# Performance work log

Measured on AMD Instinct MI355X. Metric: run time of the kernel, lower is better.

The kernel has to match this reference:

```python
import jax, jax.numpy as jnp
import numpy as np

HEADS = 8
EMBED = 128
HEAD_DIM = EMBED // HEADS


def setup_inputs() -> dict:
    key = jax.random.key(0)
    ks = jax.random.split(key, 6)
    s = 0.05
    return {
        "x": jax.random.normal(ks[0], (8, 128, 128, 128), dtype=jnp.float32),
        "Wq": jax.random.normal(ks[1], (HEAD_DIM, HEAD_DIM), dtype=jnp.float32) * s,
        "Wk": jax.random.normal(ks[2], (HEAD_DIM, HEAD_DIM), dtype=jnp.float32) * s,
        "Wv": jax.random.normal(ks[3], (HEAD_DIM, HEAD_DIM), dtype=jnp.float32) * s,
        "Wo": jax.random.normal(ks[4], (EMBED, EMBED), dtype=jnp.float32) * s,
        "bo": jnp.zeros((EMBED,), dtype=jnp.float32),
    }


def reference(x, Wq, Wk, Wv, Wo, bo):
    # is_width=False: attend along the H axis. x: [N, C, H, W]
    y = jnp.transpose(x, (0, 3, 2, 1))  # [N, W, H, C]
    N, D1, D2, C = y.shape
    y = y.reshape(N * D1, D2, HEADS, HEAD_DIM)  # [n, k, h, d]
    # nn.Linear applies y @ W.T
    q = jnp.einsum("nkhd,ed->nkhe", y, Wq)
    k = jnp.einsum("nkhd,ed->nkhe", y, Wk)
    v = jnp.einsum("nkhd,ed->nkhe", y, Wv)
    energy = jnp.einsum("nqhd,nkhd->nhqk", q, k)
    scale = jnp.asarray(EMBED, energy.dtype) ** 0.5  # note: original divides by sqrt(embed_size)
    attn = jax.nn.softmax(energy / scale, axis=-1)
    out = jnp.einsum("nhqk,nkhd->nqhd", attn, v).reshape(N, D1, D2, C)
    out = jnp.einsum("nqkc,ec->nqke", out, Wo) + bo
    return jnp.transpose(out, (0, 3, 2, 1))  # back to [N, C, H, W]
```

## Files before the change

### kernel.cpp

```cpp
#include <hip/hip_runtime.h>
#include <hip/hip_fp16.h>


typedef __attribute__((ext_vector_type(4))) float f32x4;
typedef __attribute__((ext_vector_type(4))) _Float16 f16x4;
typedef __attribute__((ext_vector_type(8))) short bf16x8;

__device__ __forceinline__ unsigned int bf16_rne(float x) {
    unsigned int u = __float_as_uint(x);
    return (u + 0x7fffu + ((u >> 16) & 1u)) >> 16;
}
__device__ __forceinline__ unsigned int pack_half2(float a, float b) {
    __half2 h = __floats2half2_rn(a, b);
    return *reinterpret_cast<unsigned int*>(&h);
}

__global__ void axattn_prep(const float* __restrict__ Wo,
                            unsigned short* __restrict__ Wob) {
    int i = blockIdx.x * 256 + threadIdx.x;
    Wob[i] = (unsigned short)bf16_rne(Wo[i]);
}

__global__ __launch_bounds__(256) void axattn_attn(
    const float* __restrict__ x,
    const float* __restrict__ Wq,
    const float* __restrict__ Wk,
    const float* __restrict__ Wv,
    unsigned short* __restrict__ AO)
{
    int bb  = blockIdx.x;
    int xcd = bb & 7;
    int kk  = bb >> 3;
    int wg  = kk & 3;
    int nh  = kk >> 2;
    int n0  = nh >> 3;
    int h   = nh & 7;
    int tid = threadIdx.x;
    int wvi = tid >> 6;
    int l   = tid & 63;
    int lr  = l & 15;
    int lg  = l >> 4;
    int w0  = xcd * 16 + wg * 4;
    int w   = w0 + wvi;

    __shared__ unsigned int xs[4 * 1280];

    #pragma unroll
    for (int it = 0; it < 4; ++it) {
        int pid = it * 256 + tid;
        int c2  = pid >> 7;
        int row = pid & 127;
        const float* gp = x + ((size_t)(n0 * 128 + h * 16 + 2 * c2) * 128 + row) * 128 + w0;
        float4 va = *(const float4*)gp;
        float4 vb = *(const float4*)(gp + 16384);
        unsigned int* dp = xs + row * 10 + c2;
        dp[0]    = pack_half2(va.x, vb.x);
        dp[1280] = pack_half2(va.y, vb.y);
        dp[2560] = pack_half2(va.z, vb.z);
        dp[3840] = pack_half2(va.w, vb.w);
    }

    const float qsc = 0.088388347648318447f * 1.4426950408889634f;
    const f32x4 zf = {0.f, 0.f, 0.f, 0.f};

    float4 wqf = *(const float4*)(Wq + lr * 16 + lg * 4);
    float4 wkf = *(const float4*)(Wk + lr * 16 + lg * 4);
    float4 wvf = *(const float4*)(Wv + lr * 16 + lg * 4);
    f16x4 fq = {(_Float16)wqf.x, (_Float16)wqf.y, (_Float16)wqf.z, (_Float16)wqf.w};
    f16x4 fk = {(_Float16)wkf.x, (_Float16)wkf.y, (_Float16)wkf.z, (_Float16)wkf.w};
    f16x4 fv = {(_Float16)wvf.x, (_Float16)wvf.y, (_Float16)wvf.z, (_Float16)wvf.w};

    __syncthreads();

    const char* yb = (const char*)xs + wvi * 5120 + lr * 40 + lg * 8;
    f16x4 yf[8];
    #pragma unroll
    for (int rt = 0; rt < 8; ++rt)
        yf[rt] = *(const f16x4*)(yb + rt * 640);

    f16x4 qb[8], ka[8], vb[8];
    #pragma unroll
    for (int t = 0; t < 8; ++t) {
        f32x4 qt = __builtin_amdgcn_mfma_f32_16x16x16f16(fq, yf[t], zf, 0, 0, 0);
        f32x4 kt = __builtin_amdgcn_mfma_f32_16x16x16f16(fk, yf[t], zf, 0, 0, 0);
        f32x4 vt = __builtin_amdgcn_mfma_f32_16x16x16f16(yf[t], fv, zf, 0, 0, 0);
        qb[t] = (f16x4){(_Float16)(qt[0] * qsc), (_Float16)(qt[1] * qsc),
                        (_Float16)(qt[2] * qsc), (_Float16)(qt[3] * qsc)};
        ka[t] = (f16x4){(_Float16)kt[0], (_Float16)kt[1], (_Float16)kt[2], (_Float16)kt[3]};
        vb[t] = (f16x4){(_Float16)vt[0], (_Float16)vt[1], (_Float16)vt[2], (_Float16)vt[3]};
    }

    unsigned short* aob = AO + ((size_t)(n0 * 128 + w) * 128 + lg * 4) * 128 + h * 16 + lr;

    #pragma unroll
    for (int qt = 0; qt < 8; ++qt) {
        f32x4 s[8];
        #pragma unroll
        for (int kt = 0; kt < 8; ++kt)
            s[kt] = __builtin_amdgcn_mfma_f32_16x16x16f16(ka[kt], qb[qt], zf, 0, 0, 0);
        float sum = 0.f;
        f16x4 pa[8];
        #pragma unroll
        for (int kt = 0; kt < 8; ++kt) {
            float p0 = __builtin_amdgcn_exp2f(s[kt][0]);
            float p1 = __builtin_amdgcn_exp2f(s[kt][1]);
            float p2 = __builtin_amdgcn_exp2f(s[kt][2]);
            float p3 = __builtin_amdgcn_exp2f(s[kt][3]);
            sum += (p0 + p1) + (p2 + p3);
            pa[kt] = (f16x4){(_Float16)p0, (_Float16)p1, (_Float16)p2, (_Float16)p3};
        }
        sum += __shfl_xor(sum, 16);
        sum += __shfl_xor(sum, 32);
        f32x4 o = zf;
        #pragma unroll
        for (int kt = 0; kt < 8; ++kt)
            o = __builtin_amdgcn_mfma_f32_16x16x16f16(pa[kt], vb[kt], o, 0, 0, 0);
        float rl = 1.f / sum;
        #pragma unroll
        for (int r = 0; r < 4; ++r) {
            float rs = __shfl(rl, lg * 4 + r);
            aob[((size_t)qt * 16 + r) * 128] = (unsigned short)bf16_rne(o[r] * rs);
        }
    }
}

__global__ __launch_bounds__(256) void axattn_proj(
    const unsigned short* __restrict__ AOb,
    const unsigned short* __restrict__ Wob,
    const float* __restrict__ bo,
    float* __restrict__ out)
{
    int bb  = blockIdx.x;
    int n0  = bb >> 7;
    int s   = bb & 127;
    int tid = threadIdx.x;
    int wv  = tid >> 6;
    int l   = tid & 63;
    int lr  = l & 15;
    int lg  = l >> 4;
    int lk  = lg * 8;
    int eb  = wv * 32;

    __shared__ char as_[128 * 272];

    #pragma unroll
    for (int it = 0; it < 8; ++it) {
        int flat = it * 256 + tid;
        int row  = flat >> 4;
        int seg  = flat & 15;
        const uint4* src = (const uint4*)(AOb + ((size_t)(n0 * 128 + row) * 128 + s) * 128) + seg;
        *(uint4*)(as_ + row * 272 + seg * 16) = *src;
    }
    __syncthreads();

    f32x4 acc[2][8];
    #pragma unroll
    for (int mi = 0; mi < 2; ++mi)
        #pragma unroll
        for (int ni = 0; ni < 8; ++ni)
            acc[mi][ni] = (f32x4){0.f, 0.f, 0.f, 0.f};

    const unsigned short* wp = Wob + (size_t)(eb + lr) * 128 + lk;

    #pragma unroll
    for (int ct = 0; ct < 4; ++ct) {
        bf16x8 a0 = *(const bf16x8*)(wp + ct * 32);
        bf16x8 a1 = *(const bf16x8*)(wp + 16 * 128 + ct * 32);
        #pragma unroll
        for (int ni = 0; ni < 8; ++ni) {
            bf16x8 b = *(const bf16x8*)(as_ + (ni * 16 + lr) * 272 + (lk + ct * 32) * 2);
            acc[0][ni] = __builtin_amdgcn_mfma_f32_16x16x32_bf16(a0, b, acc[0][ni], 0, 0, 0);
            acc[1][ni] = __builtin_amdgcn_mfma_f32_16x16x32_bf16(a1, b, acc[1][ni], 0, 0, 0);
        }
    }

    int r4 = lg * 4;
    #pragma unroll
    for (int mi = 0; mi < 2; ++mi) {
        #pragma unroll
        for (int r = 0; r < 4; ++r) {
            int e = eb + mi * 16 + r4 + r;
            float bv = bo[e];
            float* orow = out + ((size_t)(n0 * 128 + e) * 128 + s) * 128 + lr;
            #pragma unroll
            for (int ni = 0; ni < 8; ++ni)
                orow[ni * 16] = acc[mi][ni][r] + bv;
        }
    }
}

extern "C" void kernel_launch(void* const* d_in, const int* in_sizes, int n_in,
                              void* d_out, int out_size, void* d_ws, size_t ws_size,
                              hipStream_t stream) {
    const float* x  = (const float*)d_in[0];
    const float* Wq = (const float*)d_in[1];
    const float* Wk = (const float*)d_in[2];
    const float* Wv = (const float*)d_in[3];
    const float* Wo = (const float*)d_in[4];
    const float* bo = (const float*)d_in[5];
    float* out = (float*)d_out;

    unsigned short* AOb = (unsigned short*)d_ws;
    unsigned short* Wob = (unsigned short*)((char*)d_ws + (32u << 20));

    axattn_prep<<<64, 256, 0, stream>>>(Wo, Wob);
    axattn_attn<<<2048, 256, 0, stream>>>(x, Wq, Wk, Wv, AOb);
    axattn_proj<<<1024, 256, 0, stream>>>(AOb, Wob, bo, out);
}
```

Before: 158.2 us.

## Retile attention to 8-wave blocks and split projection into half-width blocks

The attention kernel now runs 512-thread blocks covering 8 consecutive w columns. Each thread loads two adjacent float4s of x, which widens the contiguous global read per row. The PV accumulation is split into two independent MFMA chains to shorten the dependency chain. The projection kernel splits each (n,s) tile into two 64-column halves and launches twice as many blocks, with Wo fragments preloaded into registers before the LDS stage. This trades more parallelism for fewer accumulators per block and extra register pressure.

```diff
diff --git a/kernel.cpp b/kernel.cpp
--- a/kernel.cpp
+++ b/kernel.cpp
@@ -21,7 +21,7 @@
     Wob[i] = (unsigned short)bf16_rne(Wo[i]);
 }
 
-__global__ __launch_bounds__(256) void axattn_attn(
+__global__ __launch_bounds__(512) void axattn_attn(
     const float* __restrict__ x,
     const float* __restrict__ Wq,
     const float* __restrict__ Wk,
@@ -30,9 +30,9 @@
 {
     int bb  = blockIdx.x;
     int xcd = bb & 7;
-    int kk  = bb >> 3;
-    int wg  = kk & 3;
-    int nh  = kk >> 2;
+    int t2  = bb >> 3;
+    int wp  = t2 & 1;
+    int nh  = t2 >> 1;
     int n0  = nh >> 3;
     int h   = nh & 7;
     int tid = threadIdx.x;
@@ -40,24 +40,28 @@
     int l   = tid & 63;
     int lr  = l & 15;
     int lg  = l >> 4;
-    int w0  = xcd * 16 + wg * 4;
+    int w0  = xcd * 16 + wp * 8;
     int w   = w0 + wvi;
 
-    __shared__ unsigned int xs[4 * 1280];
-
-    #pragma unroll
-    for (int it = 0; it < 4; ++it) {
-        int pid = it * 256 + tid;
-        int c2  = pid >> 7;
-        int row = pid & 127;
-        const float* gp = x + ((size_t)(n0 * 128 + h * 16 + 2 * c2) * 128 + row) * 128 + w0;
-        float4 va = *(const float4*)gp;
-        float4 vb = *(const float4*)(gp + 16384);
-        unsigned int* dp = xs + row * 10 + c2;
-        dp[0]    = pack_half2(va.x, vb.x);
-        dp[1280] = pack_half2(va.y, vb.y);
-        dp[2560] = pack_half2(va.z, vb.z);
-        dp[3840] = pack_half2(va.w, vb.w);
+    __shared__ unsigned int xs[8 * 1280];
+
+    {
+        int q   = tid & 1;
+        int row = (tid >> 1) & 127;
+        int c2b = tid >> 8;
+        const float* gp0 = x + ((size_t)(n0 * 128 + h * 16) * 128 + row) * 128 + w0 + q * 4;
+        #pragma unroll
+        for (int it = 0; it < 4; ++it) {
+            int c2 = it * 2 + c2b;
+            const float* gp = gp0 + (size_t)(2 * c2) * 16384;
+            float4 va = *(const float4*)gp;
+            float4 vb = *(const float4*)(gp + 16384);
+            unsigned int* dp = xs + (q * 4) * 1280 + row * 10 + c2;
+            dp[0]    = pack_half2(va.x, vb.x);
+            dp[1280] = pack_half2(va.y, vb.y);
+            dp[2560] = pack_half2(va.z, vb.z);
+            dp[3840] = pack_half2(va.w, vb.w);
+        }
     }
 
     const float qsc = 0.088388347648318447f * 1.4426950408889634f;
@@ -111,10 +115,13 @@
         }
         sum += __shfl_xor(sum, 16);
         sum += __shfl_xor(sum, 32);
-        f32x4 o = zf;
-        #pragma unroll
-        for (int kt = 0; kt < 8; ++kt)
-            o = __builtin_amdgcn_mfma_f32_16x16x16f16(pa[kt], vb[kt], o, 0, 0, 0);
+        f32x4 oA = zf, oB = zf;
+        #pragma unroll
+        for (int kt = 0; kt < 4; ++kt) {
+            oA = __builtin_amdgcn_mfma_f32_16x16x16f16(pa[kt],     vb[kt],     oA, 0, 0, 0);
+            oB = __builtin_amdgcn_mfma_f32_16x16x16f16(pa[kt + 4], vb[kt + 4], oB, 0, 0, 0);
+        }
+        f32x4 o = oA + oB;
         float rl = 1.f / sum;
         #pragma unroll
         for (int r = 0; r < 4; ++r) {
@@ -131,8 +138,9 @@
     float* __restrict__ out)
 {
     int bb  = blockIdx.x;
-    int n0  = bb >> 7;
-    int s   = bb & 127;
+    int wh  = bb & 1;
+    int s   = (bb >> 1) & 127;
+    int n0  = bb >> 8;
     int tid = threadIdx.x;
     int wv  = tid >> 6;
     int l   = tid & 63;
@@ -141,36 +149,41 @@
     int lk  = lg * 8;
     int eb  = wv * 32;
 
-    __shared__ char as_[128 * 272];
-
-    #pragma unroll
-    for (int it = 0; it < 8; ++it) {
+    __shared__ char as_[64 * 272];
+
+    const unsigned short* wp_ = Wob + (size_t)(eb + lr) * 128 + lk;
+    bf16x8 a0[4], a1[4];
+    #pragma unroll
+    for (int ct = 0; ct < 4; ++ct) {
+        a0[ct] = *(const bf16x8*)(wp_ + ct * 32);
+        a1[ct] = *(const bf16x8*)(wp_ + 16 * 128 + ct * 32);
+    }
+
+    #pragma unroll
+    for (int it = 0; it < 4; ++it) {
         int flat = it * 256 + tid;
         int row  = flat >> 4;
         int seg  = flat & 15;
-        const uint4* src = (const uint4*)(AOb + ((size_t)(n0 * 128 + row) * 128 + s) * 128) + seg;
+        const uint4* src = (const uint4*)(AOb
+            + ((size_t)(n0 * 128 + wh * 64 + row) * 128 + s) * 128) + seg;
         *(uint4*)(as_ + row * 272 + seg * 16) = *src;
     }
     __syncthreads();
 
-    f32x4 acc[2][8];
+    f32x4 acc[2][4];
     #pragma unroll
     for (int mi = 0; mi < 2; ++mi)
         #pragma unroll
-        for (int ni = 0; ni < 8; ++ni)
+        for (int ni = 0; ni < 4; ++ni)
             acc[mi][ni] = (f32x4){0.f, 0.f, 0.f, 0.f};
 
-    const unsigned short* wp = Wob + (size_t)(eb + lr) * 128 + lk;
-
     #pragma unroll
     for (int ct = 0; ct < 4; ++ct) {
-        bf16x8 a0 = *(const bf16x8*)(wp + ct * 32);
-        bf16x8 a1 = *(const bf16x8*)(wp + 16 * 128 + ct * 32);
-        #pragma unroll
-        for (int ni = 0; ni < 8; ++ni) {
+        #pragma unroll
+        for (int ni = 0; ni < 4; ++ni) {
             bf16x8 b = *(const bf16x8*)(as_ + (ni * 16 + lr) * 272 + (lk + ct * 32) * 2);
-            acc[0][ni] = __builtin_amdgcn_mfma_f32_16x16x32_bf16(a0, b, acc[0][ni], 0, 0, 0);
-            acc[1][ni] = __builtin_amdgcn_mfma_f32_16x16x32_bf16(a1, b, acc[1][ni], 0, 0, 0);
+            acc[0][ni] = __builtin_amdgcn_mfma_f32_16x16x32_bf16(a0[ct], b, acc[0][ni], 0, 0, 0);
+            acc[1][ni] = __builtin_amdgcn_mfma_f32_16x16x32_bf16(a1[ct], b, acc[1][ni], 0, 0, 0);
         }
     }
 
@@ -181,9 +194,9 @@
         for (int r = 0; r < 4; ++r) {
             int e = eb + mi * 16 + r4 + r;
             float bv = bo[e];
-            float* orow = out + ((size_t)(n0 * 128 + e) * 128 + s) * 128 + lr;
+            float* orow = out + ((size_t)(n0 * 128 + e) * 128 + s) * 128 + wh * 64 + lr;
             #pragma unroll
-            for (int ni = 0; ni < 8; ++ni)
+            for (int ni = 0; ni < 4; ++ni)
                 orow[ni * 16] = acc[mi][ni][r] + bv;
         }
     }
@@ -204,6 +217,6 @@
     unsigned short* Wob = (unsigned short*)((char*)d_ws + (32u << 20));
 
     axattn_prep<<<64, 256, 0, stream>>>(Wo, Wob);
-    axattn_attn<<<2048, 256, 0, stream>>>(x, Wq, Wk, Wv, AOb);
-    axattn_proj<<<1024, 256, 0, stream>>>(AOb, Wob, bo, out);
-}
+    axattn_attn<<<1024, 512, 0, stream>>>(x, Wq, Wk, Wv, AOb);
+    axattn_proj<<<2048, 256, 0, stream>>>(AOb, Wob, bo, out);
+}
```

Measured after the change: 154.7 us. 1.02x faster.
